# Kernel tuning notes

Hardware: AMD Instinct MI355X
Metric: run time of the kernel (lower is better)

The kernel has to match this reference:

```python
import jax, jax.numpy as jnp
import numpy as np


def conv2d(x, w, b, pad=0, groups=1):
    y = jax.lax.conv_general_dilated(
        x, w, (1, 1), [(pad, pad), (pad, pad)],
        dimension_numbers=('NCHW', 'OIHW', 'NCHW'), feature_group_count=groups)
    return y + b[None, :, None, None]


def layernorm(x, w, b, eps=1e-5):
    # per-pixel LayerNorm over channel dim (matches to_3d -> nn.LayerNorm(dim) -> to_4d)
    mu = x.mean(1, keepdims=True)
    var = ((x - mu) ** 2).mean(1, keepdims=True)
    return (x - mu) * jax.lax.rsqrt(var + eps) * w[None, :, None, None] + b[None, :, None, None]


def setup_inputs():
    key = jax.random.key(0)
    ks = jax.random.split(key, 16)
    B, C, H, W = 1, 64, 64, 64
    heads, dh = 8, 8
    inner = heads * dh          # 64
    hid_lc = 32                 # max(16, inner // 2)
    hid_f = 4 * C               # 256, ffn_expansion_factor = 4
    def s(k, shape, fan):
        return (jax.random.normal(k, shape, jnp.float32) / np.float32(np.sqrt(fan)))
    return {
        'x': jax.random.normal(ks[0], (B, C, H, W), jnp.float32),
        'luma': jax.random.uniform(ks[1], (B, 1, H, W), jnp.float32),
        'ln1_w': jnp.ones((C,), jnp.float32), 'ln1_b': jnp.zeros((C,), jnp.float32),
        'qkv_w': s(ks[2], (3 * inner, C, 1, 1), C), 'qkv_b': jnp.zeros((3 * inner,), jnp.float32),
        'proj_w': s(ks[3], (C, inner, 1, 1), inner), 'proj_b': jnp.zeros((C,), jnp.float32),
        'lc1_w': s(ks[4], (hid_lc, 1, 3, 3), 9), 'lc1_b': jnp.zeros((hid_lc,), jnp.float32),
        'lc2_w': s(ks[5], (hid_lc, hid_lc, 3, 3), 9 * hid_lc), 'lc2_b': jnp.zeros((hid_lc,), jnp.float32),
        'gam_w': s(ks[6], (inner, hid_lc, 1, 1), hid_lc), 'gam_b': jnp.zeros((inner,), jnp.float32),
        'bet_w': s(ks[7], (inner, hid_lc, 1, 1), hid_lc), 'bet_b': jnp.zeros((inner,), jnp.float32),
        'alpha': jnp.float32(0.1),
        'ln2_w': jnp.ones((C,), jnp.float32), 'ln2_b': jnp.zeros((C,), jnp.float32),
        'ffn1_w': s(ks[8], (hid_f, C, 1, 1), C), 'ffn1_b': jnp.zeros((hid_f,), jnp.float32),
        'dw_w': s(ks[9], (hid_f, 1, 3, 3), 9), 'dw_b': jnp.zeros((hid_f,), jnp.float32),
        'ffn2_w': s(ks[10], (C, hid_f, 1, 1), hid_f), 'ffn2_b': jnp.zeros((C,), jnp.float32),
    }


def reference(x, luma, ln1_w, ln1_b, qkv_w, qkv_b, proj_w, proj_b,
              lc1_w, lc1_b, lc2_w, lc2_b, gam_w, gam_b, bet_w, bet_b, alpha,
              ln2_w, ln2_b, ffn1_w, ffn1_b, dw_w, dw_b, ffn2_w, ffn2_b):
    B, C, H, W = x.shape
    heads = 8
    N = H * W
    # --- attention branch ---
    xn = layernorm(x, ln1_w, ln1_b)
    qkv = conv2d(xn, qkv_w, qkv_b)             # [B, 3*inner, H, W]
    inner = qkv.shape[1] // 3
    dh = inner // heads

    def to_bhnd(t):  # b (h d) x y -> b h (x y) d
        return t.reshape(B, heads, dh, N).transpose(0, 1, 3, 2)

    q, k, v = [to_bhnd(t) for t in jnp.split(qkv, 3, axis=1)]
    # luma conditioning
    h1 = jax.nn.relu(conv2d(luma, lc1_w, lc1_b, pad=1))
    h1 = jax.nn.relu(conv2d(h1, lc2_w, lc2_b, pad=1))
    g = to_bhnd(conv2d(h1, gam_w, gam_b))
    bt = to_bhnd(conv2d(h1, bet_w, bet_b))
    q = g * q + bt
    k = g * k + bt
    v = g * v + bt
    # additive luma bias on q (avg_pool2d 3x3, count_include_pad=True -> fixed /9)
    invL = 1.0 - luma
    invL = jax.lax.reduce_window(invL, 0.0, jax.lax.add, (1, 1, 3, 3), (1, 1, 1, 1),
                                 [(0, 0), (0, 0), (1, 1), (1, 1)]) / 9.0
    invL = invL.reshape(B, N)
    invL = invL - invL.mean(-1, keepdims=True)
    q = q + alpha * invL[:, None, :, None]
    scale = dh ** -0.5
    attn = jax.nn.softmax(jnp.einsum('bhid,bhjd->bhij', q, k) * scale, axis=-1)
    out = jnp.einsum('bhij,bhjd->bhid', attn, v)
    out = out.transpose(0, 1, 3, 2).reshape(B, inner, H, W)
    x = x + conv2d(out, proj_w, proj_b)
    # --- ConvFFN branch ---
    y = layernorm(x, ln2_w, ln2_b)
    y = conv2d(y, ffn1_w, ffn1_b)
    y = conv2d(y, dw_w, dw_b, pad=1, groups=y.shape[1])
    y = jax.nn.gelu(y, approximate=False)
    y = conv2d(y, ffn2_w, ffn2_b)
    return x + y
```

## Files before the change

### kernel.cpp

```cpp
#include <hip/hip_runtime.h>
#include <math.h>

#define NPIX 4096
#define IMG 64

typedef __attribute__((ext_vector_type(8))) short bf16x8;
typedef __attribute__((ext_vector_type(4))) float floatx4;
typedef __attribute__((ext_vector_type(4))) unsigned int uintx4;

__device__ __forceinline__ unsigned int split_pack(float x) {
  unsigned int u = __float_as_uint(x);
  unsigned int hif = u & 0xffff0000u;
  float lof = x - __uint_as_float(hif);
  return (u >> 16) | (__float_as_uint(lof) & 0xffff0000u);
}

__device__ __forceinline__ unsigned int hi_pair(float a, float b) {
  return (__float_as_uint(a) >> 16) | (__float_as_uint(b) & 0xffff0000u);
}

__global__ __launch_bounds__(256) void lc1_kernel(
    const float* __restrict__ luma, const float* __restrict__ w1,
    const float* __restrict__ b1, float* __restrict__ h1,
    float* __restrict__ pooled, float* __restrict__ bsums,
    unsigned short* __restrict__ cbuf) {
  __shared__ float red[256];
  int tile = blockIdx.x, ocg = blockIdx.y;
  int tid = threadIdx.x;
  if (tile == 0 && ocg == 0 && tid < 16) cbuf[tid] = (tid < 8) ? 0x3F80 : 0;
  int p = tile * 256 + tid;
  int py = p >> 6, px = p & 63;
  float v[9];
#pragma unroll
  for (int dy = 0; dy < 3; dy++)
#pragma unroll
    for (int dx = 0; dx < 3; dx++) {
      int y = py + dy - 1, x = px + dx - 1;
      v[dy * 3 + dx] =
          (y >= 0 && y < IMG && x >= 0 && x < IMG) ? luma[y * IMG + x] : 0.f;
    }
#pragma unroll
  for (int o = 0; o < 4; o++) {
    int oc = ocg * 4 + o;
    float s = b1[oc];
#pragma unroll
    for (int t = 0; t < 9; t++) s = fmaf(w1[oc * 9 + t], v[t], s);
    h1[oc * NPIX + p] = fmaxf(s, 0.f);
  }
  if (ocg == 0) {
    float sv = 0.f;
#pragma unroll
    for (int t = 0; t < 9; t++) sv += v[t];
    float cy = 3.f - (py == 0 ? 1.f : 0.f) - (py == 63 ? 1.f : 0.f);
    float cx = 3.f - (px == 0 ? 1.f : 0.f) - (px == 63 ? 1.f : 0.f);
    float pv = (cy * cx - sv) * (1.f / 9.f);
    pooled[p] = pv;
    red[tid] = pv;
    __syncthreads();
    for (int st = 128; st > 0; st >>= 1) {
      if (tid < st) red[tid] += red[tid + st];
      __syncthreads();
    }
    if (tid == 0) bsums[tile] = red[0];
  }
}

__global__ __launch_bounds__(256) void lc2_kernel(
    const float* __restrict__ h1, const float* __restrict__ w2,
    const float* __restrict__ b2, float* __restrict__ h2) {
  __shared__ float tin[32][324];
  __shared__ float swt[4][32][9];
  int tile = blockIdx.x, ocg = blockIdx.y;
  int ty0 = (tile >> 2) * 16, tx0 = (tile & 3) * 16;
  int tid = threadIdx.x;
  for (int idx = tid; idx < 32 * 324; idx += 256) {
    int ic = idx / 324, pos = idx - ic * 324;
    int py = pos / 18, px = pos - py * 18;
    int gy = ty0 + py - 1, gx = tx0 + px - 1;
    tin[ic][pos] = (gy >= 0 && gy < IMG && gx >= 0 && gx < IMG)
                       ? h1[ic * NPIX + gy * IMG + gx]
                       : 0.f;
  }
  for (int idx = tid; idx < 4 * 32 * 9; idx += 256) {
    int o = idx / 288, r = idx - o * 288;
    swt[o][r / 9][r % 9] = w2[(ocg * 4 + o) * 288 + r];
  }
  __syncthreads();
  int ly = tid >> 4, lx = tid & 15;
  int p = (ty0 + ly) * IMG + tx0 + lx;
  float acc[4];
#pragma unroll
  for (int o = 0; o < 4; o++) acc[o] = b2[ocg * 4 + o];
  for (int ic = 0; ic < 32; ic++) {
    float v[9];
#pragma unroll
    for (int dy = 0; dy < 3; dy++)
#pragma unroll
      for (int dx = 0; dx < 3; dx++)
        v[dy * 3 + dx] = tin[ic][(ly + dy) * 18 + lx + dx];
#pragma unroll
    for (int o = 0; o < 4; o++)
#pragma unroll
      for (int t = 0; t < 9; t++) acc[o] = fmaf(swt[o][ic][t], v[t], acc[o]);
  }
#pragma unroll
  for (int o = 0; o < 4; o++)
    h2[(ocg * 4 + o) * NPIX + p] = fmaxf(acc[o], 0.f);
}

__global__ __launch_bounds__(256) void ln_qkv_kernel(
    const float* __restrict__ X, const float* __restrict__ lnw,
    const float* __restrict__ lnb, const float* __restrict__ W,
    const float* __restrict__ bias, const float* __restrict__ gamW,
    const float* __restrict__ gamB, const float* __restrict__ betW,
    const float* __restrict__ betB, const float* __restrict__ h2,
    const float* __restrict__ pooled, const float* __restrict__ bsums,
    const float* __restrict__ alpha, unsigned short* __restrict__ qhl,
    unsigned short* __restrict__ khl, unsigned short* __restrict__ vthx,
    unsigned short* __restrict__ vtlx) {
  const float QSCALE = 0.35355339059327376f * 1.4426950408889634f;
  __shared__ float xs[64][64];
  __shared__ float wsh[64][64];
  __shared__ float h2s[32][64];
  __shared__ float wgs[32][64];
  __shared__ float wbs[32][64];
  __shared__ float psum[4][64];
  __shared__ float mu[64];
  __shared__ float rs[64];
  int n0 = blockIdx.x * 64, part = blockIdx.y, m0 = part * 64;
  int tid = threadIdx.x;
  int c = tid >> 2, pg = (tid & 3) * 16;
  {
    const float4* src = (const float4*)&X[c * NPIX + n0 + pg];
    float4* dst = (float4*)&xs[c][pg];
    dst[0] = src[0]; dst[1] = src[1]; dst[2] = src[2]; dst[3] = src[3];
  }
  {
    int m = tid >> 2, kg = (tid & 3) * 16;
    const float4* wr = (const float4*)&W[(m0 + m) * 64 + kg];
    float4 w0 = wr[0], w1 = wr[1], w2 = wr[2], w3 = wr[3];
    float wv[16] = {w0.x, w0.y, w0.z, w0.w, w1.x, w1.y, w1.z, w1.w,
                    w2.x, w2.y, w2.z, w2.w, w3.x, w3.y, w3.z, w3.w};
#pragma unroll
    for (int j = 0; j < 16; j++) wsh[kg + j][m] = wv[j];
  }
  {
    int i0 = tid * 2;
    int k = i0 >> 4, nf = (i0 & 15) * 4;
    *(float4*)&h2s[k][nf] = *(const float4*)&h2[k * NPIX + n0 + nf];
    int i1 = i0 + 1;
    int k1 = i1 >> 4, nf1 = (i1 & 15) * 4;
    *(float4*)&h2s[k1][nf1] = *(const float4*)&h2[k1 * NPIX + n0 + nf1];
  }
  {
    int m = tid >> 2, kg = (tid & 3) * 8;
    const float4* g0 = (const float4*)&gamW[m * 32 + kg];
    float4 a = g0[0], b4 = g0[1];
    float gv[8] = {a.x, a.y, a.z, a.w, b4.x, b4.y, b4.z, b4.w};
#pragma unroll
    for (int j = 0; j < 8; j++) wgs[kg + j][m] = gv[j];
    const float4* bb0 = (const float4*)&betW[m * 32 + kg];
    float4 c4 = bb0[0], d4 = bb0[1];
    float bv[8] = {c4.x, c4.y, c4.z, c4.w, d4.x, d4.y, d4.z, d4.w};
#pragma unroll
    for (int j = 0; j < 8; j++) wbs[kg + j][m] = bv[j];
  }
  __syncthreads();
  int px = tid & 63, qq = tid >> 6;
  float s = 0.f;
#pragma unroll
  for (int cc = 0; cc < 16; cc++) s += xs[qq * 16 + cc][px];
  psum[qq][px] = s;
  __syncthreads();
  if (tid < 64) {
    float t = psum[0][tid] + psum[1][tid] + psum[2][tid] + psum[3][tid];
    mu[tid] = t * (1.f / 64.f);
  }
  __syncthreads();
  float mm = mu[px];
  s = 0.f;
#pragma unroll
  for (int cc = 0; cc < 16; cc++) {
    float d = xs[qq * 16 + cc][px] - mm;
    s = fmaf(d, d, s);
  }
  psum[qq][px] = s;
  __syncthreads();
  if (tid < 64) {
    float t = psum[0][tid] + psum[1][tid] + psum[2][tid] + psum[3][tid];
    rs[tid] = rsqrtf(t * (1.f / 64.f) + 1e-5f);
  }
  __syncthreads();
  {
    float wc = lnw[c], bc = lnb[c];
#pragma unroll
    for (int j = 0; j < 16; j++) {
      int p = pg + j;
      xs[c][p] = (xs[c][p] - mu[p]) * rs[p] * wc + bc;
    }
  }
  __syncthreads();
  int tx = tid & 15, ty = tid >> 4;
  float ga[4][4] = {}, ba[4][4] = {};
#pragma unroll 8
  for (int kk = 0; kk < 32; kk++) {
    float4 wg4 = *(const float4*)&wgs[kk][ty * 4];
    float4 wb4 = *(const float4*)&wbs[kk][ty * 4];
    float4 h24 = *(const float4*)&h2s[kk][tx * 4];
    float gv[4] = {wg4.x, wg4.y, wg4.z, wg4.w};
    float bv[4] = {wb4.x, wb4.y, wb4.z, wb4.w};
    float hv[4] = {h24.x, h24.y, h24.z, h24.w};
#pragma unroll
    for (int im = 0; im < 4; im++)
#pragma unroll
      for (int in = 0; in < 4; in++) {
        ga[im][in] = fmaf(gv[im], hv[in], ga[im][in]);
        ba[im][in] = fmaf(bv[im], hv[in], ba[im][in]);
      }
  }
#pragma unroll
  for (int im = 0; im < 4; im++) {
    int cc = ty * 4 + im;
    float gb = gamB[cc], bb2 = betB[cc];
#pragma unroll
    for (int in = 0; in < 4; in++) {
      ga[im][in] += gb;
      ba[im][in] += bb2;
    }
  }
  float acc[4][4] = {};
#pragma unroll 8
  for (int kk = 0; kk < 64; kk++) {
    float4 a = *(const float4*)&wsh[kk][ty * 4];
    float4 b4 = *(const float4*)&xs[kk][tx * 4];
    float av[4] = {a.x, a.y, a.z, a.w};
    float bv[4] = {b4.x, b4.y, b4.z, b4.w};
#pragma unroll
    for (int im = 0; im < 4; im++)
#pragma unroll
      for (int in = 0; in < 4; in++)
        acc[im][in] = fmaf(av[im], bv[in], acc[im][in]);
  }
  float val[4][4];
#pragma unroll
  for (int im = 0; im < 4; im++) {
    int cc = ty * 4 + im;
    float bv = bias[m0 + cc];
#pragma unroll
    for (int in = 0; in < 4; in++)
      val[im][in] = fmaf(ga[im][in], acc[im][in] + bv, ba[im][in]);
  }
  if (part == 0) {
    float msum = 0.f;
#pragma unroll
    for (int t = 0; t < 16; t++) msum += bsums[t];
    float mean = msum * (1.f / 4096.f);
    float a0 = alpha[0];
    const float4 pv = *(const float4*)&pooled[n0 + tx * 4];
    float iv[4] = {a0 * (pv.x - mean), a0 * (pv.y - mean),
                   a0 * (pv.z - mean), a0 * (pv.w - mean)};
#pragma unroll
    for (int im = 0; im < 4; im++)
#pragma unroll
      for (int in = 0; in < 4; in++)
        val[im][in] = (val[im][in] + iv[in]) * QSCALE;
  }
  if (part < 2) {
    unsigned short* dst = (part == 0) ? qhl : khl;
    int h = ty >> 1, d0 = (ty & 1) * 4;
#pragma unroll
    for (int in = 0; in < 4; in++) {
      int n = n0 + tx * 4 + in;
      unsigned int pk[4];
#pragma unroll
      for (int im = 0; im < 4; im++) pk[im] = split_pack(val[im][in]);
      short4 hi, lo;
      hi.x = (short)(pk[0] & 0xffffu); hi.y = (short)(pk[1] & 0xffffu);
      hi.z = (short)(pk[2] & 0xffffu); hi.w = (short)(pk[3] & 0xffffu);
      lo.x = (short)(pk[0] >> 16); lo.y = (short)(pk[1] >> 16);
      lo.z = (short)(pk[2] >> 16); lo.w = (short)(pk[3] >> 16);
      unsigned short* base = dst + ((size_t)(h * NPIX + n) << 4) + d0;
      *(short4*)base = hi;
      *(short4*)(base + 8) = lo;
    }
  } else {
    int nq = n0 + tx * 4;
    int off0 = (nq >> 5) * 32 + ((nq >> 4) & 1) * 4 + ((nq >> 2) & 3) * 8;
#pragma unroll
    for (int im = 0; im < 4; im++) {
      int cc = ty * 4 + im;
      unsigned int pk[4];
#pragma unroll
      for (int in = 0; in < 4; in++) pk[in] = split_pack(val[im][in]);
      short4 hi, lo;
      hi.x = (short)(pk[0] & 0xffffu); hi.y = (short)(pk[1] & 0xffffu);
      hi.z = (short)(pk[2] & 0xffffu); hi.w = (short)(pk[3] & 0xffffu);
      lo.x = (short)(pk[0] >> 16); lo.y = (short)(pk[1] >> 16);
      lo.z = (short)(pk[2] >> 16); lo.w = (short)(pk[3] >> 16);
      *(short4*)(vthx + (size_t)cc * NPIX + off0) = hi;
      *(short4*)(vtlx + (size_t)cc * NPIX + off0) = lo;
    }
  }
}

__global__ __launch_bounds__(256, 4) void attn_kernel(
    const unsigned short* __restrict__ qhl,
    const unsigned short* __restrict__ khl,
    const unsigned short* __restrict__ vthx,
    const unsigned short* __restrict__ vtlx,
    const unsigned short* __restrict__ cbuf, float* __restrict__ pacc,
    float* __restrict__ pl) {
  int tid = threadIdx.x;
  int wave = tid >> 6, lane = tid & 63;
  int g = lane >> 4, c = lane & 15;
  int h = blockIdx.y, jp = blockIdx.z;
  int i0 = blockIdx.x * 128 + wave * 32;
  int jbase = jp * 1024;
  const bf16x8 qB0 = *(const bf16x8*)(qhl + ((size_t)(h * NPIX + i0 + c) << 4) +
                                      ((g & 1) << 3));
  const bf16x8 qB1 = *(const bf16x8*)(
      qhl + ((size_t)(h * NPIX + i0 + 16 + c) << 4) + ((g & 1) << 3));
  const unsigned short* kp =
      khl + ((size_t)(h * NPIX + jbase + c) << 4) + ((g >> 1) << 3);
  const unsigned short* vhp;
  const unsigned short* vlp;
  int vstep;
  if (c < 8) {
    vhp = vthx + (size_t)(h * 8 + c) * NPIX + jbase + (g << 3);
    vlp = vtlx + (size_t)(h * 8 + c) * NPIX + jbase + (g << 3);
    vstep = 32;
  } else {
    vhp = (c == 8) ? cbuf : (cbuf + 8);
    vlp = cbuf + 8;
    vstep = 0;
  }
  floatx4 zero4 = {0.f, 0.f, 0.f, 0.f};
  floatx4 aH0 = zero4, aM0 = zero4, aH1 = zero4, aM1 = zero4;
#pragma unroll 2
  for (int jt = 0; jt < 32; ++jt) {
    bf16x8 ka0 = *(const bf16x8*)kp;
    bf16x8 ka1 = *(const bf16x8*)(kp + 256);
    bf16x8 avh = *(const bf16x8*)vhp;
    bf16x8 avl = *(const bf16x8*)vlp;
    kp += 512;
    vhp += vstep;
    vlp += vstep;
    floatx4 s00 =
        __builtin_amdgcn_mfma_f32_16x16x32_bf16(ka0, qB0, zero4, 0, 0, 0);
    floatx4 s01 =
        __builtin_amdgcn_mfma_f32_16x16x32_bf16(ka1, qB0, zero4, 0, 0, 0);
    floatx4 s10 =
        __builtin_amdgcn_mfma_f32_16x16x32_bf16(ka0, qB1, zero4, 0, 0, 0);
    floatx4 s11 =
        __builtin_amdgcn_mfma_f32_16x16x32_bf16(ka1, qB1, zero4, 0, 0, 0);
    {
      float p0 = __builtin_amdgcn_exp2f(fminf(s00[0], 80.f));
      float p1 = __builtin_amdgcn_exp2f(fminf(s00[1], 80.f));
      float p2 = __builtin_amdgcn_exp2f(fminf(s00[2], 80.f));
      float p3 = __builtin_amdgcn_exp2f(fminf(s00[3], 80.f));
      float p4 = __builtin_amdgcn_exp2f(fminf(s01[0], 80.f));
      float p5 = __builtin_amdgcn_exp2f(fminf(s01[1], 80.f));
      float p6 = __builtin_amdgcn_exp2f(fminf(s01[2], 80.f));
      float p7 = __builtin_amdgcn_exp2f(fminf(s01[3], 80.f));
      uintx4 bh;
      bh.x = hi_pair(p0, p1);
      bh.y = hi_pair(p2, p3);
      bh.z = hi_pair(p4, p5);
      bh.w = hi_pair(p6, p7);
      bf16x8 pbh = __builtin_bit_cast(bf16x8, bh);
      aH0 = __builtin_amdgcn_mfma_f32_16x16x32_bf16(avh, pbh, aH0, 0, 0, 0);
      aM0 = __builtin_amdgcn_mfma_f32_16x16x32_bf16(avl, pbh, aM0, 0, 0, 0);
    }
    {
      float p0 = __builtin_amdgcn_exp2f(fminf(s10[0], 80.f));
      float p1 = __builtin_amdgcn_exp2f(fminf(s10[1], 80.f));
      float p2 = __builtin_amdgcn_exp2f(fminf(s10[2], 80.f));
      float p3 = __builtin_amdgcn_exp2f(fminf(s10[3], 80.f));
      float p4 = __builtin_amdgcn_exp2f(fminf(s11[0], 80.f));
      float p5 = __builtin_amdgcn_exp2f(fminf(s11[1], 80.f));
      float p6 = __builtin_amdgcn_exp2f(fminf(s11[2], 80.f));
      float p7 = __builtin_amdgcn_exp2f(fminf(s11[3], 80.f));
      uintx4 bh;
      bh.x = hi_pair(p0, p1);
      bh.y = hi_pair(p2, p3);
      bh.z = hi_pair(p4, p5);
      bh.w = hi_pair(p6, p7);
      bf16x8 pbh = __builtin_bit_cast(bf16x8, bh);
      aH1 = __builtin_amdgcn_mfma_f32_16x16x32_bf16(avh, pbh, aH1, 0, 0, 0);
      aM1 = __builtin_amdgcn_mfma_f32_16x16x32_bf16(avl, pbh, aM1, 0, 0, 0);
    }
  }
  floatx4 o0 = aH0 + aM0;
  floatx4 o1 = aH1 + aM1;
  if (g < 2) {
    size_t b0 = (size_t)((jp * 8 + h) * NPIX + i0 + c);
    *(float4*)&pacc[b0 * 8 + g * 4] = make_float4(o0[0], o0[1], o0[2], o0[3]);
    size_t b1 = b0 + 16;
    *(float4*)&pacc[b1 * 8 + g * 4] = make_float4(o1[0], o1[1], o1[2], o1[3]);
  } else if (g == 2) {
    pl[(size_t)((jp * 8 + h) * NPIX + i0 + c)] = o0[0];
    pl[(size_t)((jp * 8 + h) * NPIX + i0 + 16 + c)] = o1[0];
  }
}

__global__ __launch_bounds__(256) void proj_ffn1_kernel(
    const float* __restrict__ pacc, const float* __restrict__ pl,
    const float* __restrict__ Wp, const float* __restrict__ bp,
    const float* __restrict__ x, const float* __restrict__ ln2w,
    const float* __restrict__ ln2b, const float* __restrict__ W1,
    const float* __restrict__ b1f, float* __restrict__ x1,
    float* __restrict__ f1) {
  __shared__ float at[64][33];
  __shared__ float wsh[64][64];
  __shared__ float xsl[64][33];
  __shared__ float ps[8][33];
  __shared__ float pq[8][33];
  __shared__ float mus[32];
  __shared__ float rss[32];
  int n0 = blockIdx.x * 32;
  int ch = blockIdx.y;
  int tid = threadIdx.x;
  {
    int mm = tid >> 2, kg = (tid & 3) * 16;
    const float4* wr = (const float4*)&Wp[mm * 64 + kg];
    float4 w0 = wr[0], w1 = wr[1], w2 = wr[2], w3 = wr[3];
    float wv[16] = {w0.x, w0.y, w0.z, w0.w, w1.x, w1.y, w1.z, w1.w,
                    w2.x, w2.y, w2.z, w2.w, w3.x, w3.y, w3.z, w3.w};
#pragma unroll
    for (int j = 0; j < 16; j++) wsh[kg + j][mm] = wv[j];
  }
  {
    int hh = tid >> 5, nn = tid & 31;
    int i = n0 + nn;
    float L = 0.f, o[8] = {};
#pragma unroll
    for (int p = 0; p < 4; p++) {
      size_t base = (size_t)((p * 8 + hh) * NPIX + i);
      L += pl[base];
      const float4 a0 = *(const float4*)&pacc[base * 8];
      const float4 a1 = *(const float4*)&pacc[base * 8 + 4];
      o[0] += a0.x; o[1] += a0.y; o[2] += a0.z; o[3] += a0.w;
      o[4] += a1.x; o[5] += a1.y; o[6] += a1.z; o[7] += a1.w;
    }
    float inv = 1.f / L;
#pragma unroll
    for (int d = 0; d < 8; d++) at[hh * 8 + d][nn] = o[d] * inv;
  }
  __syncthreads();
  int ty = tid >> 5, tx = tid & 31;
  float acc[8] = {};
#pragma unroll 8
  for (int k = 0; k < 64; k++) {
    float b = at[k][tx];
    float4 a0 = *(const float4*)&wsh[k][ty * 8];
    float4 a1 = *(const float4*)&wsh[k][ty * 8 + 4];
    acc[0] = fmaf(a0.x, b, acc[0]);
    acc[1] = fmaf(a0.y, b, acc[1]);
    acc[2] = fmaf(a0.z, b, acc[2]);
    acc[3] = fmaf(a0.w, b, acc[3]);
    acc[4] = fmaf(a1.x, b, acc[4]);
    acc[5] = fmaf(a1.y, b, acc[5]);
    acc[6] = fmaf(a1.z, b, acc[6]);
    acc[7] = fmaf(a1.w, b, acc[7]);
  }
  float v[8], sn = 0.f, qn = 0.f;
#pragma unroll
  for (int im = 0; im < 8; im++) {
    int row = ty * 8 + im;
    float vv = acc[im] + bp[row] + x[row * NPIX + n0 + tx];
    v[im] = vv;
    sn += vv;
    qn = fmaf(vv, vv, qn);
  }
  if (ch == 0) {
#pragma unroll
    for (int im = 0; im < 8; im++)
      x1[(ty * 8 + im) * NPIX + n0 + tx] = v[im];
  }
  ps[ty][tx] = sn;
  pq[ty][tx] = qn;
  __syncthreads();
  if (tid < 32) {
    float s = 0.f, q = 0.f;
#pragma unroll
    for (int t = 0; t < 8; t++) {
      s += ps[t][tid];
      q += pq[t][tid];
    }
    float mu = s * (1.f / 64.f);
    mus[tid] = mu;
    rss[tid] = rsqrtf(q * (1.f / 64.f) - mu * mu + 1e-5f);
  }
  __syncthreads();
  {
    float muv = mus[tx], rsv = rss[tx];
#pragma unroll
    for (int im = 0; im < 8; im++) {
      int row = ty * 8 + im;
      xsl[row][tx] = (v[im] - muv) * rsv * ln2w[row] + ln2b[row];
    }
  }
  {
    int mm = tid >> 2, kg = (tid & 3) * 16;
    const float4* wr = (const float4*)&W1[(ch * 64 + mm) * 64 + kg];
    float4 w0 = wr[0], w1 = wr[1], w2 = wr[2], w3 = wr[3];
    float wv[16] = {w0.x, w0.y, w0.z, w0.w, w1.x, w1.y, w1.z, w1.w,
                    w2.x, w2.y, w2.z, w2.w, w3.x, w3.y, w3.z, w3.w};
#pragma unroll
    for (int j = 0; j < 16; j++) wsh[kg + j][mm] = wv[j];
  }
  __syncthreads();
  float a2[8] = {};
#pragma unroll 8
  for (int k = 0; k < 64; k++) {
    float b = xsl[k][tx];
    float4 a0 = *(const float4*)&wsh[k][ty * 8];
    float4 a1 = *(const float4*)&wsh[k][ty * 8 + 4];
    a2[0] = fmaf(a0.x, b, a2[0]);
    a2[1] = fmaf(a0.y, b, a2[1]);
    a2[2] = fmaf(a0.z, b, a2[2]);
    a2[3] = fmaf(a0.w, b, a2[3]);
    a2[4] = fmaf(a1.x, b, a2[4]);
    a2[5] = fmaf(a1.y, b, a2[5]);
    a2[6] = fmaf(a1.z, b, a2[6]);
    a2[7] = fmaf(a1.w, b, a2[7]);
  }
#pragma unroll
  for (int im = 0; im < 8; im++) {
    int row = ch * 64 + ty * 8 + im;
    f1[row * NPIX + n0 + tx] = a2[im] + b1f[row];
  }
}

__global__ __launch_bounds__(256) void dw_gelu_kernel(
    const float* __restrict__ f1, const float* __restrict__ w,
    const float* __restrict__ b, float* __restrict__ f2) {
  int t = blockIdx.x * 256 + threadIdx.x;
  int c = t >> 10, pq = t & 1023;
  int py = pq >> 4, px0 = (pq & 15) << 2;
  const float* base = f1 + c * NPIX;
  float wv[9];
#pragma unroll
  for (int i = 0; i < 9; i++) wv[i] = w[c * 9 + i];
  float bc = b[c];
  float a[4] = {bc, bc, bc, bc};
#pragma unroll
  for (int dy = 0; dy < 3; dy++) {
    int y = py + dy - 1;
    if (y < 0 || y > 63) continue;
    const float* row = base + y * IMG + px0;
    float4 mid = *(const float4*)row;
    float left = (px0 > 0) ? row[-1] : 0.f;
    float right = (px0 < 60) ? row[4] : 0.f;
    float win[6] = {left, mid.x, mid.y, mid.z, mid.w, right};
#pragma unroll
    for (int o = 0; o < 4; o++)
#pragma unroll
      for (int dx = 0; dx < 3; dx++)
        a[o] = fmaf(wv[dy * 3 + dx], win[o + dx], a[o]);
  }
  float4 o4;
  float* op = &o4.x;
#pragma unroll
  for (int o = 0; o < 4; o++)
    op[o] = 0.5f * a[o] * (1.f + erff(a[o] * 0.70710678118654752f));
  *(float4*)&f2[c * NPIX + py * IMG + px0] = o4;
}

__global__ __launch_bounds__(256) void gemm16_kernel(
    const float* __restrict__ W, const float* __restrict__ X,
    const float* __restrict__ bias, const float* __restrict__ resid,
    float* __restrict__ C, int K) {
  __shared__ float xs[32][64];
  __shared__ float wsh[32][16];
  int n0 = blockIdx.x * 64, m0 = blockIdx.y * 16;
  int tid = threadIdx.x;
  int m = tid >> 4, ng = tid & 15;
  float acc[4] = {};
  for (int k0 = 0; k0 < K; k0 += 32) {
    {
      int i0 = tid * 2;
      int k = i0 >> 4, nf = (i0 & 15) * 4;
      *(float4*)&xs[k][nf] = *(const float4*)&X[(k0 + k) * NPIX + n0 + nf];
      int i1 = i0 + 1;
      int k1 = i1 >> 4, nf1 = (i1 & 15) * 4;
      *(float4*)&xs[k1][nf1] = *(const float4*)&X[(k0 + k1) * NPIX + n0 + nf1];
    }
#pragma unroll
    for (int e = tid; e < 512; e += 256) {
      int mm = e >> 5, kk = e & 31;
      wsh[kk][mm] = W[(m0 + mm) * K + k0 + kk];
    }
    __syncthreads();
#pragma unroll 8
    for (int kk = 0; kk < 32; kk++) {
      float a = wsh[kk][m];
      float4 b4 = *(const float4*)&xs[kk][ng * 4];
      acc[0] = fmaf(a, b4.x, acc[0]);
      acc[1] = fmaf(a, b4.y, acc[1]);
      acc[2] = fmaf(a, b4.z, acc[2]);
      acc[3] = fmaf(a, b4.w, acc[3]);
    }
    __syncthreads();
  }
  int row = m0 + m;
  float bv = bias[row];
  float4 o = make_float4(acc[0] + bv, acc[1] + bv, acc[2] + bv, acc[3] + bv);
  const float4 r4 = *(const float4*)&resid[row * NPIX + n0 + ng * 4];
  o.x += r4.x; o.y += r4.y; o.z += r4.z; o.w += r4.w;
  *(float4*)&C[row * NPIX + n0 + ng * 4] = o;
}

extern "C" void kernel_launch(void* const* d_in, const int* in_sizes, int n_in,
                              void* d_out, int out_size, void* d_ws,
                              size_t ws_size, hipStream_t stream) {
  const float* x      = (const float*)d_in[0];
  const float* luma   = (const float*)d_in[1];
  const float* ln1_w  = (const float*)d_in[2];
  const float* ln1_b  = (const float*)d_in[3];
  const float* qkv_w  = (const float*)d_in[4];
  const float* qkv_b  = (const float*)d_in[5];
  const float* proj_w = (const float*)d_in[6];
  const float* proj_b = (const float*)d_in[7];
  const float* lc1_w  = (const float*)d_in[8];
  const float* lc1_b  = (const float*)d_in[9];
  const float* lc2_w  = (const float*)d_in[10];
  const float* lc2_b  = (const float*)d_in[11];
  const float* gam_w  = (const float*)d_in[12];
  const float* gam_b  = (const float*)d_in[13];
  const float* bet_w  = (const float*)d_in[14];
  const float* bet_b  = (const float*)d_in[15];
  const float* alpha  = (const float*)d_in[16];
  const float* ln2_w  = (const float*)d_in[17];
  const float* ln2_b  = (const float*)d_in[18];
  const float* ffn1_w = (const float*)d_in[19];
  const float* ffn1_b = (const float*)d_in[20];
  const float* dw_w   = (const float*)d_in[21];
  const float* dw_b   = (const float*)d_in[22];
  const float* ffn2_w = (const float*)d_in[23];
  const float* ffn2_b = (const float*)d_in[24];
  float* out = (float*)d_out;

  float* w = (float*)d_ws;
  float* pooled = w + 0;
  float* bsums  = w + 4096;
  unsigned short* cbuf = (unsigned short*)(w + 4160);
  unsigned short* qhl  = (unsigned short*)(w + 4224);
  unsigned short* khl  = (unsigned short*)(w + 266368);
  unsigned short* vthx = (unsigned short*)(w + 528512);
  unsigned short* vtlx = (unsigned short*)(w + 659584);
  float* pacc = w + 790656;
  float* pl   = w + 1839232;
  float* x1   = w + 1970304;
  float* f1   = w + 2232448;
  float* f2   = w + 3281024;
  float* h2   = w + 4329600;
  float* h1   = w + 4460672;

  lc1_kernel<<<dim3(16, 8), 256, 0, stream>>>(luma, lc1_w, lc1_b, h1, pooled,
                                              bsums, cbuf);
  lc2_kernel<<<dim3(16, 8), 256, 0, stream>>>(h1, lc2_w, lc2_b, h2);
  ln_qkv_kernel<<<dim3(64, 3), 256, 0, stream>>>(
      x, ln1_w, ln1_b, qkv_w, qkv_b, gam_w, gam_b, bet_w, bet_b, h2, pooled,
      bsums, alpha, qhl, khl, vthx, vtlx);
  attn_kernel<<<dim3(32, 8, 4), 256, 0, stream>>>(qhl, khl, vthx, vtlx, cbuf,
                                                  pacc, pl);
  proj_ffn1_kernel<<<dim3(128, 4), 256, 0, stream>>>(
      pacc, pl, proj_w, proj_b, x, ln2_w, ln2_b, ffn1_w, ffn1_b, x1, f1);
  dw_gelu_kernel<<<1024, 256, 0, stream>>>(f1, dw_w, dw_b, f2);
  gemm16_kernel<<<dim3(64, 4), 256, 0, stream>>>(ffn2_w, f2, ffn2_b, x1, out,
                                                 256);
}
```

Measured before the change: 203.1 us.

## Split attention keys across 8 partitions and precompute LN1 stats in lc2

The attention kernel now splits the key dimension into 8 chunks of 512 instead of 4 chunks of 1024, doubling the grid so more blocks run concurrently, and raises the occupancy hint in launch bounds. The projection kernel reduces 8 partial accumulators instead of 4. LayerNorm-1 mean and inverse std are computed once per pixel in the lc2 kernel's first channel group, using a one-pass variance, and read by ln_qkv_kernel, removing several block syncs and reductions that were repeated in all three qkv partitions. The trade-offs are more partial-sum traffic, tighter register limits in attention, and slightly less numerically stable variance.

```diff
diff --git a/kernel.cpp b/kernel.cpp
--- a/kernel.cpp
+++ b/kernel.cpp
@@ -67,7 +67,8 @@
 
 __global__ __launch_bounds__(256) void lc2_kernel(
     const float* __restrict__ h1, const float* __restrict__ w2,
-    const float* __restrict__ b2, float* __restrict__ h2) {
+    const float* __restrict__ b2, const float* __restrict__ x,
+    float* __restrict__ h2, float* __restrict__ mu1, float* __restrict__ rs1) {
   __shared__ float tin[32][324];
   __shared__ float swt[4][32][9];
   int tile = blockIdx.x, ocg = blockIdx.y;
@@ -106,10 +107,23 @@
 #pragma unroll
   for (int o = 0; o < 4; o++)
     h2[(ocg * 4 + o) * NPIX + p] = fmaxf(acc[o], 0.f);
+  if (ocg == 0) {
+    float s = 0.f, q = 0.f;
+#pragma unroll 8
+    for (int cc = 0; cc < 64; cc++) {
+      float xv = x[cc * NPIX + p];
+      s += xv;
+      q = fmaf(xv, xv, q);
+    }
+    float mu = s * (1.f / 64.f);
+    mu1[p] = mu;
+    rs1[p] = rsqrtf(q * (1.f / 64.f) - mu * mu + 1e-5f);
+  }
 }
 
 __global__ __launch_bounds__(256) void ln_qkv_kernel(
-    const float* __restrict__ X, const float* __restrict__ lnw,
+    const float* __restrict__ X, const float* __restrict__ mu1,
+    const float* __restrict__ rs1, const float* __restrict__ lnw,
     const float* __restrict__ lnb, const float* __restrict__ W,
     const float* __restrict__ bias, const float* __restrict__ gamW,
     const float* __restrict__ gamB, const float* __restrict__ betW,
@@ -124,12 +138,15 @@
   __shared__ float h2s[32][64];
   __shared__ float wgs[32][64];
   __shared__ float wbs[32][64];
-  __shared__ float psum[4][64];
   __shared__ float mu[64];
   __shared__ float rs[64];
   int n0 = blockIdx.x * 64, part = blockIdx.y, m0 = part * 64;
   int tid = threadIdx.x;
   int c = tid >> 2, pg = (tid & 3) * 16;
+  if (tid < 64) {
+    mu[tid] = mu1[n0 + tid];
+    rs[tid] = rs1[n0 + tid];
+  }
   {
     const float4* src = (const float4*)&X[c * NPIX + n0 + pg];
     float4* dst = (float4*)&xs[c][pg];
@@ -164,31 +181,6 @@
     float bv[8] = {c4.x, c4.y, c4.z, c4.w, d4.x, d4.y, d4.z, d4.w};
 #pragma unroll
     for (int j = 0; j < 8; j++) wbs[kg + j][m] = bv[j];
-  }
-  __syncthreads();
-  int px = tid & 63, qq = tid >> 6;
-  float s = 0.f;
-#pragma unroll
-  for (int cc = 0; cc < 16; cc++) s += xs[qq * 16 + cc][px];
-  psum[qq][px] = s;
-  __syncthreads();
-  if (tid < 64) {
-    float t = psum[0][tid] + psum[1][tid] + psum[2][tid] + psum[3][tid];
-    mu[tid] = t * (1.f / 64.f);
-  }
-  __syncthreads();
-  float mm = mu[px];
-  s = 0.f;
-#pragma unroll
-  for (int cc = 0; cc < 16; cc++) {
-    float d = xs[qq * 16 + cc][px] - mm;
-    s = fmaf(d, d, s);
-  }
-  psum[qq][px] = s;
-  __syncthreads();
-  if (tid < 64) {
-    float t = psum[0][tid] + psum[1][tid] + psum[2][tid] + psum[3][tid];
-    rs[tid] = rsqrtf(t * (1.f / 64.f) + 1e-5f);
   }
   __syncthreads();
   {
@@ -303,7 +295,7 @@
   }
 }
 
-__global__ __launch_bounds__(256, 4) void attn_kernel(
+__global__ __launch_bounds__(256, 6) void attn_kernel(
     const unsigned short* __restrict__ qhl,
     const unsigned short* __restrict__ khl,
     const unsigned short* __restrict__ vthx,
@@ -315,7 +307,7 @@
   int g = lane >> 4, c = lane & 15;
   int h = blockIdx.y, jp = blockIdx.z;
   int i0 = blockIdx.x * 128 + wave * 32;
-  int jbase = jp * 1024;
+  int jbase = jp * 512;
   const bf16x8 qB0 = *(const bf16x8*)(qhl + ((size_t)(h * NPIX + i0 + c) << 4) +
                                       ((g & 1) << 3));
   const bf16x8 qB1 = *(const bf16x8*)(
@@ -337,7 +329,7 @@
   floatx4 zero4 = {0.f, 0.f, 0.f, 0.f};
   floatx4 aH0 = zero4, aM0 = zero4, aH1 = zero4, aM1 = zero4;
 #pragma unroll 2
-  for (int jt = 0; jt < 32; ++jt) {
+  for (int jt = 0; jt < 16; ++jt) {
     bf16x8 ka0 = *(const bf16x8*)kp;
     bf16x8 ka1 = *(const bf16x8*)(kp + 256);
     bf16x8 avh = *(const bf16x8*)vhp;
@@ -434,7 +426,7 @@
     int i = n0 + nn;
     float L = 0.f, o[8] = {};
 #pragma unroll
-    for (int p = 0; p < 4; p++) {
+    for (int p = 0; p < 8; p++) {
       size_t base = (size_t)((p * 8 + hh) * NPIX + i);
       L += pl[base];
       const float4 a0 = *(const float4*)&pacc[base * 8];
@@ -645,25 +637,28 @@
   float* pooled = w + 0;
   float* bsums  = w + 4096;
   unsigned short* cbuf = (unsigned short*)(w + 4160);
-  unsigned short* qhl  = (unsigned short*)(w + 4224);
-  unsigned short* khl  = (unsigned short*)(w + 266368);
-  unsigned short* vthx = (unsigned short*)(w + 528512);
-  unsigned short* vtlx = (unsigned short*)(w + 659584);
-  float* pacc = w + 790656;
-  float* pl   = w + 1839232;
-  float* x1   = w + 1970304;
-  float* f1   = w + 2232448;
-  float* f2   = w + 3281024;
-  float* h2   = w + 4329600;
-  float* h1   = w + 4460672;
+  float* mu1 = w + 4224;
+  float* rs1 = w + 8320;
+  unsigned short* qhl  = (unsigned short*)(w + 12416);
+  unsigned short* khl  = (unsigned short*)(w + 274560);
+  unsigned short* vthx = (unsigned short*)(w + 536704);
+  unsigned short* vtlx = (unsigned short*)(w + 667776);
+  float* pacc = w + 798848;
+  float* pl   = w + 2896000;
+  float* x1   = w + 3158144;
+  float* f1   = w + 3420288;
+  float* f2   = w + 4468864;
+  float* h2   = w + 5517440;
+  float* h1   = w + 5648512;
 
   lc1_kernel<<<dim3(16, 8), 256, 0, stream>>>(luma, lc1_w, lc1_b, h1, pooled,
                                               bsums, cbuf);
-  lc2_kernel<<<dim3(16, 8), 256, 0, stream>>>(h1, lc2_w, lc2_b, h2);
+  lc2_kernel<<<dim3(16, 8), 256, 0, stream>>>(h1, lc2_w, lc2_b, x, h2, mu1,
+                                              rs1);
   ln_qkv_kernel<<<dim3(64, 3), 256, 0, stream>>>(
-      x, ln1_w, ln1_b, qkv_w, qkv_b, gam_w, gam_b, bet_w, bet_b, h2, pooled,
-      bsums, alpha, qhl, khl, vthx, vtlx);
-  attn_kernel<<<dim3(32, 8, 4), 256, 0, stream>>>(qhl, khl, vthx, vtlx, cbuf,
+      x, mu1, rs1, ln1_w, ln1_b, qkv_w, qkv_b, gam_w, gam_b, bet_w, bet_b, h2,
+      pooled, bsums, alpha, qhl, khl, vthx, vtlx);
+  attn_kernel<<<dim3(32, 8, 8), 256, 0, stream>>>(qhl, khl, vthx, vtlx, cbuf,
                                                   pacc, pl);
   proj_ffn1_kernel<<<dim3(128, 4), 256, 0, stream>>>(
       pacc, pl, proj_w, proj_b, x, ln2_w, ln2_b, ffn1_w, ffn1_b, x1, f1);
```

Result: no change. 205.9 us (+1.3%).
